# Optimization experiments

Measured on AMD Instinct MI355X. Metric: run time of the kernel, lower is better.

The kernel has to match this reference:

```python
import jax, jax.numpy as jnp
import numpy as np

N_NODES = 100000
N_EDGES = 1600000
IN_C, HID_C, OUT_C = 128, 256, 128


def setup_inputs() -> dict:
    key = jax.random.key(0)
    ks = jax.random.split(key, 6)
    x = jax.random.normal(ks[0], (N_NODES, IN_C), dtype=jnp.float32)
    edge_index = jax.random.randint(ks[1], (2, N_EDGES), 0, N_NODES, dtype=jnp.int64)
    s = 0.05
    W1a = jax.random.normal(ks[2], (IN_C, HID_C), dtype=jnp.float32) * s
    b1a = jnp.zeros((HID_C,), dtype=jnp.float32)
    W2a = jax.random.normal(ks[3], (HID_C, HID_C), dtype=jnp.float32) * s
    b2a = jnp.zeros((HID_C,), dtype=jnp.float32)
    W1b = jax.random.normal(ks[4], (HID_C, HID_C), dtype=jnp.float32) * s
    b1b = jnp.zeros((HID_C,), dtype=jnp.float32)
    W2b = jax.random.normal(ks[5], (HID_C, OUT_C), dtype=jnp.float32) * s
    b2b = jnp.zeros((OUT_C,), dtype=jnp.float32)
    return {"x": x, "edge_index": edge_index, "W1a": W1a, "b1a": b1a,
            "W2a": W2a, "b2a": b2a, "W1b": W1b, "b1b": b1b,
            "W2b": W2b, "b2b": b2b}


def _gin_conv(x, src, dst, W1, b1, W2, b2):
    # GINConv (eps=0): nn( x + sum_{j in N(i)} x_j )
    agg = jax.ops.segment_sum(x[src], dst, num_segments=N_NODES)  # [N, d]
    h = x + agg
    h = jnp.maximum(h @ W1 + b1, 0.0)
    return h @ W2 + b2


def reference(x, edge_index, W1a, b1a, W2a, b2a, W1b, b1b, W2b, b2b):
    src, dst = edge_index[0], edge_index[1]
    h = jnp.maximum(_gin_conv(x, src, dst, W1a, b1a, W2a, b2a), 0.0)  # relu(conv1)
    # dropout is identity in eval mode
    out = _gin_conv(h, src, dst, W1b, b1b, W2b, b2b)  # conv2
    return out
```

## Files before the change

kernel.cpp:

```cpp
#include <hip/hip_runtime.h>


#define N_NODES 100000
#define N_EDGES 1600000
#define NBUCK 13

typedef unsigned short ushort_t;
typedef short bf16x8 __attribute__((ext_vector_type(8)));
typedef float floatx4 __attribute__((ext_vector_type(4)));

static __device__ __forceinline__ ushort_t f2bf(float f) {
    unsigned u = __float_as_uint(f);
    u = (u + 0x7FFFu + ((u >> 16) & 1u)) >> 16;
    return (ushort_t)u;
}
static __device__ __forceinline__ unsigned pack2bf(float lo, float hi) {
    return (unsigned)f2bf(lo) | ((unsigned)f2bf(hi) << 16);
}
static __device__ __forceinline__ void addu4(float* acc, const uint4 v) {
    const unsigned w0 = v.x, w1 = v.y, w2 = v.z, w3 = v.w;
    acc[0] += __uint_as_float(w0 << 16);
    acc[1] += __uint_as_float(w0 & 0xFFFF0000u);
    acc[2] += __uint_as_float(w1 << 16);
    acc[3] += __uint_as_float(w1 & 0xFFFF0000u);
    acc[4] += __uint_as_float(w2 << 16);
    acc[5] += __uint_as_float(w2 & 0xFFFF0000u);
    acc[6] += __uint_as_float(w3 << 16);
    acc[7] += __uint_as_float(w3 & 0xFFFF0000u);
}

__global__ __launch_bounds__(256) void cvt_x_kernel(const float* __restrict__ X,
                                                    ushort_t* __restrict__ Xb, int n8) {
    int i = blockIdx.x * 256 + threadIdx.x;
    if (i < n8) {
        const float4 a = ((const float4*)X)[2 * i];
        const float4 b = ((const float4*)X)[2 * i + 1];
        uint4 r;
        r.x = pack2bf(a.x, a.y);
        r.y = pack2bf(a.z, a.w);
        r.z = pack2bf(b.x, b.y);
        r.w = pack2bf(b.z, b.w);
        ((uint4*)Xb)[i] = r;
    }
}

__global__ __launch_bounds__(256) void cvt_all_kernel(
    const float* __restrict__ W1a, const float* __restrict__ W2a,
    const float* __restrict__ W1b, const float* __restrict__ W2b,
    ushort_t* __restrict__ wt1a, ushort_t* __restrict__ wt2a,
    ushort_t* __restrict__ wt1b, ushort_t* __restrict__ wt2b) {
    int i = blockIdx.x * 256 + threadIdx.x;
    if (i < 32768) {
        int k = i >> 8, n = i & 255;
        wt1a[n * 128 + k] = f2bf(W1a[i]);
    } else if (i < 98304) {
        int j = i - 32768, k = j >> 8, n = j & 255;
        wt2a[n * 256 + k] = f2bf(W2a[j]);
    } else if (i < 163840) {
        int j = i - 98304, k = j >> 8, n = j & 255;
        wt1b[n * 256 + k] = f2bf(W1b[j]);
    } else if (i < 196608) {
        int j = i - 163840, k = j >> 7, n = j & 127;
        wt2b[n * 256 + k] = f2bf(W2b[j]);
    }
}

__global__ __launch_bounds__(256) void hist_kernel(const int* __restrict__ src,
                                                   const int* __restrict__ dst,
                                                   int* __restrict__ deg, int nE) {
    const int bucket = blockIdx.y;
    for (int e = blockIdx.x * 256 + threadIdx.x; e < nE; e += gridDim.x * 256) {
        int d = dst[e];
        int s = src[e];
        if ((unsigned)d < (unsigned)N_NODES && (unsigned)s < (unsigned)N_NODES &&
            (d >> 13) == bucket)
            atomicAdd(&deg[d], 1);
    }
}

__global__ __launch_bounds__(256) void fill_kernel(const int* __restrict__ src,
                                                   const int* __restrict__ dst,
                                                   int* __restrict__ cursor,
                                                   int* __restrict__ csr_src, int nE) {
    const int bucket = blockIdx.y;
    for (int e = blockIdx.x * 256 + threadIdx.x; e < nE; e += gridDim.x * 256) {
        int d = dst[e];
        int s = src[e];
        if ((unsigned)d < (unsigned)N_NODES && (unsigned)s < (unsigned)N_NODES &&
            (d >> 13) == bucket) {
            int pos = atomicAdd(&cursor[d], 1);
            csr_src[pos] = s;
        }
    }
}

__global__ __launch_bounds__(256) void scan1_kernel(const int* __restrict__ deg,
                                                    int* __restrict__ bsum, int n) {
    __shared__ int l[256];
    int b = blockIdx.x, t = threadIdx.x;
    int base = b * 1024 + t * 4;
    int s = 0;
#pragma unroll
    for (int k = 0; k < 4; ++k) {
        int i = base + k;
        if (i < n) s += deg[i];
    }
    l[t] = s;
    __syncthreads();
    for (int off = 128; off > 0; off >>= 1) {
        if (t < off) l[t] += l[t + off];
        __syncthreads();
    }
    if (t == 0) bsum[b] = l[0];
}

__global__ __launch_bounds__(128) void scan2_kernel(const int* __restrict__ bsum,
                                                    int* __restrict__ boff, int nb) {
    __shared__ int l[128];
    int t = threadIdx.x;
    int v = (t < nb) ? bsum[t] : 0;
    l[t] = v;
    __syncthreads();
    for (int off = 1; off < 128; off <<= 1) {
        int add = (t >= off) ? l[t - off] : 0;
        __syncthreads();
        l[t] += add;
        __syncthreads();
    }
    if (t < nb) boff[t] = l[t] - v;
}

__global__ __launch_bounds__(256) void scan3_kernel(const int* __restrict__ deg,
                                                    const int* __restrict__ boff,
                                                    int* __restrict__ row_ptr,
                                                    int* __restrict__ cursor, int n) {
    __shared__ int l[256];
    int b = blockIdx.x, t = threadIdx.x;
    int base = b * 1024 + t * 4;
    int d[4];
    int s = 0;
#pragma unroll
    for (int k = 0; k < 4; ++k) {
        int i = base + k;
        d[k] = (i < n) ? deg[i] : 0;
        s += d[k];
    }
    l[t] = s;
    __syncthreads();
    for (int off = 1; off < 256; off <<= 1) {
        int add = (t >= off) ? l[t - off] : 0;
        __syncthreads();
        l[t] += add;
        __syncthreads();
    }
    int run = boff[b] + l[t] - s;
#pragma unroll
    for (int k = 0; k < 4; ++k) {
        int i = base + k;
        if (i < n) {
            row_ptr[i] = run;
            cursor[i] = run;
        }
        run += d[k];
    }
}

template <int C>
__global__ __launch_bounds__(256) void agg_gather_kernel(
    const ushort_t* __restrict__ X, ushort_t* __restrict__ T,
    const int* __restrict__ row_ptr, const int* __restrict__ deg,
    const int* __restrict__ csr_src, int nN) {
    constexpr int G = C / 8;
    constexpr int NPW = 64 / G;
    const int lane = threadIdx.x & 63;
    const int wid = threadIdx.x >> 6;
    const int node = blockIdx.x * 4 + wid;
    if (node >= nN) return;
    const int sub = lane / G;
    const size_t coff = (size_t)(lane % G) * 8;

    float acc[8];
#pragma unroll
    for (int k = 0; k < 8; ++k) acc[k] = 0.f;

    const int base = row_ptr[node];
    const int dg = deg[node];
    for (int j0 = 0; j0 < dg; j0 += 64) {
        int cnt = dg - j0;
        if (cnt > 64) cnt = 64;
        int nidx = 0;
        if (lane < cnt) nidx = csr_src[base + j0 + lane];
        if ((unsigned)nidx >= (unsigned)N_NODES) nidx = 0;
        int j = 0;
        for (; j + 4 * NPW <= cnt; j += 4 * NPW) {
            uint4 v[4];
#pragma unroll
            for (int u = 0; u < 4; ++u) {
                int idx = __shfl(nidx, j + u * NPW + sub);
                v[u] = *(const uint4*)(X + (size_t)idx * C + coff);
            }
#pragma unroll
            for (int u = 0; u < 4; ++u) addu4(acc, v[u]);
        }
        for (; j < cnt; j += NPW) {
            int jj = j + sub;
            int srcl = (jj < cnt) ? jj : (cnt - 1);
            int idx = __shfl(nidx, srcl);
            if (jj < cnt) {
                uint4 v = *(const uint4*)(X + (size_t)idx * C + coff);
                addu4(acc, v);
            }
        }
    }
    if (sub == 0) {
        uint4 v = *(const uint4*)(X + (size_t)node * C + coff);
        addu4(acc, v);
    }
#pragma unroll
    for (int off = G; off < 64; off <<= 1)
#pragma unroll
        for (int k = 0; k < 8; ++k) acc[k] += __shfl_xor(acc[k], off);

    if (lane < G) {
        uint4 r;
        r.x = pack2bf(acc[0], acc[1]);
        r.y = pack2bf(acc[2], acc[3]);
        r.z = pack2bf(acc[4], acc[5]);
        r.w = pack2bf(acc[6], acc[7]);
        *(uint4*)(T + (size_t)node * C + coff) = r;
    }
}

template <bool RELU, typename OT>
__global__ __launch_bounds__(256) void gemm_kernel(
    const ushort_t* A, const ushort_t* __restrict__ Wt,
    const float* __restrict__ bias, OT* C, int M, int N, int K) {
    constexpr int BM = 128, BN = 128, BK = 32;
    constexpr int LDW = BK + 8;
    __shared__ ushort_t As[BM * LDW];
    __shared__ ushort_t Bs[BN * LDW];

    const int tid = threadIdx.x;
    const int lane = tid & 63;
    const int wid = tid >> 6;
    const int wm = wid & 1;
    const int wn = wid >> 1;
    const int l15 = lane & 15;
    const int q = lane >> 4;

    const int bm = blockIdx.x * BM;
    const int bn = blockIdx.y * BN;

    floatx4 acc[4][4];
#pragma unroll
    for (int mi = 0; mi < 4; ++mi)
#pragma unroll
        for (int ni = 0; ni < 4; ++ni) {
            floatx4 z = {0.f, 0.f, 0.f, 0.f};
            acc[mi][ni] = z;
        }

    for (int kt = 0; kt < K; kt += BK) {
#pragma unroll
        for (int p = 0; p < 4; ++p) {
            int i = p * 256 + tid;
            int row = i >> 3;
            int c4 = i & 7;
            int gr = bm + row;
            if (gr > M - 1) gr = M - 1;
            ushort4 u = *(const ushort4*)(A + (size_t)gr * K + kt + c4 * 4);
            *(ushort4*)&As[row * LDW + c4 * 4] = u;
        }
#pragma unroll
        for (int p = 0; p < 4; ++p) {
            int i = p * 256 + tid;
            int row = i >> 3;
            int c4 = i & 7;
            ushort4 u = *(const ushort4*)(Wt + (size_t)(bn + row) * K + kt + c4 * 4);
            *(ushort4*)&Bs[row * LDW + c4 * 4] = u;
        }
        __syncthreads();

        bf16x8 av[4], bv[4];
#pragma unroll
        for (int mi = 0; mi < 4; ++mi)
            av[mi] = *(const bf16x8*)&As[(wm * 64 + mi * 16 + l15) * LDW + q * 8];
#pragma unroll
        for (int ni = 0; ni < 4; ++ni)
            bv[ni] = *(const bf16x8*)&Bs[(wn * 64 + ni * 16 + l15) * LDW + q * 8];
#pragma unroll
        for (int mi = 0; mi < 4; ++mi)
#pragma unroll
            for (int ni = 0; ni < 4; ++ni)
                acc[mi][ni] = __builtin_amdgcn_mfma_f32_16x16x32_bf16(
                    av[mi], bv[ni], acc[mi][ni], 0, 0, 0);
        __syncthreads();
    }

    float bval[4];
#pragma unroll
    for (int ni = 0; ni < 4; ++ni) bval[ni] = bias[bn + wn * 64 + ni * 16 + l15];
#pragma unroll
    for (int mi = 0; mi < 4; ++mi) {
#pragma unroll
        for (int r = 0; r < 4; ++r) {
            int row = bm + wm * 64 + mi * 16 + q * 4 + r;
            if (row < M) {
#pragma unroll
                for (int ni = 0; ni < 4; ++ni) {
                    int col = bn + wn * 64 + ni * 16 + l15;
                    float v = acc[mi][ni][r] + bval[ni];
                    if (RELU) v = v > 0.f ? v : 0.f;
                    if constexpr (sizeof(OT) == 2)
                        C[(size_t)row * N + col] = f2bf(v);
                    else
                        C[(size_t)row * N + col] = v;
                }
            }
        }
    }
}

extern "C" void kernel_launch(void* const* d_in, const int* in_sizes, int n_in,
                              void* d_out, int out_size, void* d_ws, size_t ws_size,
                              hipStream_t stream) {
    const float* x   = (const float*)d_in[0];
    const int*   ei  = (const int*)d_in[1];
    const float* W1a = (const float*)d_in[2];
    const float* b1a = (const float*)d_in[3];
    const float* W2a = (const float*)d_in[4];
    const float* b2a = (const float*)d_in[5];
    const float* W1b = (const float*)d_in[6];
    const float* b1b = (const float*)d_in[7];
    const float* W2b = (const float*)d_in[8];
    const float* b2b = (const float*)d_in[9];
    const int* src = ei;
    const int* dst = ei + N_EDGES;
    float* out = (float*)d_out;

    char* base = (char*)d_ws;
    size_t o = 0;
    ushort_t* wt1a = (ushort_t*)(base + o); o += 128 * 256 * 2;
    ushort_t* wt2a = (ushort_t*)(base + o); o += 256 * 256 * 2;
    ushort_t* wt1b = (ushort_t*)(base + o); o += 256 * 256 * 2;
    ushort_t* wt2b = (ushort_t*)(base + o); o += 256 * 128 * 2;
    o = (o + 255) & ~(size_t)255;
    int* deg     = (int*)(base + o); o += (size_t)N_NODES * 4;
    int* row_ptr = (int*)(base + o); o += (size_t)N_NODES * 4;
    int* cursor  = (int*)(base + o); o += (size_t)N_NODES * 4;
    int* bsum    = (int*)(base + o); o += 128 * 4;
    int* boff    = (int*)(base + o); o += 128 * 4;
    o = (o + 255) & ~(size_t)255;
    int* csr_src = (int*)(base + o); o += (size_t)N_EDGES * 4;
    o = (o + 255) & ~(size_t)255;
    ushort_t* t1   = (ushort_t*)(base + o); o += (size_t)N_NODES * 128 * 2;
    ushort_t* tbig = (ushort_t*)(base + o); o += (size_t)N_NODES * 256 * 2;
    (void)ws_size; (void)o; (void)in_sizes; (void)n_in; (void)out_size;

    ushort_t* inter = (ushort_t*)d_out;
    ushort_t* xb    = (ushort_t*)d_out;

    cvt_all_kernel<<<768, 256, 0, stream>>>(W1a, W2a, W1b, W2b,
                                            wt1a, wt2a, wt1b, wt2b);
    cvt_x_kernel<<<(N_NODES * 128 / 8 + 255) / 256, 256, 0, stream>>>(
        x, xb, N_NODES * 128 / 8);

    const int NB = (N_NODES + 1023) / 1024;
    hipMemsetAsync(deg, 0, (size_t)N_NODES * 4, stream);
    hist_kernel<<<dim3(1024, NBUCK), 256, 0, stream>>>(src, dst, deg, N_EDGES);
    scan1_kernel<<<NB, 256, 0, stream>>>(deg, bsum, N_NODES);
    scan2_kernel<<<1, 128, 0, stream>>>(bsum, boff, NB);
    scan3_kernel<<<NB, 256, 0, stream>>>(deg, boff, row_ptr, cursor, N_NODES);
    fill_kernel<<<dim3(1024, NBUCK), 256, 0, stream>>>(src, dst, cursor, csr_src,
                                                       N_EDGES);

    const int gm = (N_NODES + 127) / 128;
    const int ga = (N_NODES + 3) / 4;

    agg_gather_kernel<128><<<ga, 256, 0, stream>>>(xb, t1, row_ptr, deg,
                                                   csr_src, N_NODES);
    gemm_kernel<true, ushort_t><<<dim3(gm, 2), 256, 0, stream>>>(
        t1, wt1a, b1a, tbig, N_NODES, 256, 128);
    gemm_kernel<true, ushort_t><<<dim3(gm, 2), 256, 0, stream>>>(
        tbig, wt2a, b2a, inter, N_NODES, 256, 256);

    agg_gather_kernel<256><<<ga, 256, 0, stream>>>(inter, tbig, row_ptr,
                                                   deg, csr_src, N_NODES);
    gemm_kernel<true, ushort_t><<<dim3(gm, 2), 256, 0, stream>>>(
        tbig, wt1b, b1b, inter, N_NODES, 256, 256);
    gemm_kernel<false, float><<<dim3(gm, 1), 256, 0, stream>>>(
        inter, wt2b, b2b, out, N_NODES, 128, 256);
}
```

Before: 590.8 us.

## Use direct global-to-LDS loads in GEMM and predicated zero-row gather unrolling

The GEMM tile loads now use global_load_lds (16-byte direct global-to-LDS transfers) with an unpadded LDS layout. This removes the register round-trip and the ds_write instructions but gives up the padding that avoided bank conflicts on the MFMA fragment reads. The aggregation kernel drops its tail loop: out-of-range neighbors read from a zeroed dummy row, and the unroll factor is a template parameter (4 for 128 channels, 8 for 256). Together these aim for more loads in flight per wave, at the cost of some wasted loads on low-degree nodes.

```diff
diff --git a/kernel.cpp b/kernel.cpp
--- a/kernel.cpp
+++ b/kernel.cpp
@@ -28,6 +28,11 @@
     acc[6] += __uint_as_float(w3 << 16);
     acc[7] += __uint_as_float(w3 & 0xFFFF0000u);
 }
+
+#define GLOAD_LDS16(g, l)                                                     \
+    __builtin_amdgcn_global_load_lds(                                         \
+        (const __attribute__((address_space(1))) void*)(g),                   \
+        (__attribute__((address_space(3))) void*)(l), 16, 0, 0)
 
 __global__ __launch_bounds__(256) void cvt_x_kernel(const float* __restrict__ X,
                                                     ushort_t* __restrict__ Xb, int n8) {
@@ -165,19 +170,20 @@
     }
 }
 
-template <int C>
+template <int C, int U>
 __global__ __launch_bounds__(256) void agg_gather_kernel(
     const ushort_t* __restrict__ X, ushort_t* __restrict__ T,
     const int* __restrict__ row_ptr, const int* __restrict__ deg,
-    const int* __restrict__ csr_src, int nN) {
+    const int* __restrict__ csr_src, const ushort_t* __restrict__ zrow, int nN) {
     constexpr int G = C / 8;
     constexpr int NPW = 64 / G;
+    constexpr int B = U * NPW;
     const int lane = threadIdx.x & 63;
     const int wid = threadIdx.x >> 6;
     const int node = blockIdx.x * 4 + wid;
     if (node >= nN) return;
     const int sub = lane / G;
-    const size_t coff = (size_t)(lane % G) * 8;
+    const int coff = (lane % G) * 8;
 
     float acc[8];
 #pragma unroll
@@ -188,28 +194,20 @@
     for (int j0 = 0; j0 < dg; j0 += 64) {
         int cnt = dg - j0;
         if (cnt > 64) cnt = 64;
-        int nidx = 0;
-        if (lane < cnt) nidx = csr_src[base + j0 + lane];
+        int nidx = (lane < cnt) ? csr_src[base + j0 + lane] : 0;
         if ((unsigned)nidx >= (unsigned)N_NODES) nidx = 0;
-        int j = 0;
-        for (; j + 4 * NPW <= cnt; j += 4 * NPW) {
-            uint4 v[4];
-#pragma unroll
-            for (int u = 0; u < 4; ++u) {
-                int idx = __shfl(nidx, j + u * NPW + sub);
-                v[u] = *(const uint4*)(X + (size_t)idx * C + coff);
+        for (int j = 0; j < cnt; j += B) {
+            uint4 v[U];
+#pragma unroll
+            for (int u = 0; u < U; ++u) {
+                int jj = j + u * NPW + sub;
+                bool ok = jj < cnt;
+                int idx = __shfl(nidx, ok ? jj : 0);
+                const ushort_t* p = ok ? (X + (size_t)idx * C) : zrow;
+                v[u] = *(const uint4*)(p + coff);
             }
 #pragma unroll
-            for (int u = 0; u < 4; ++u) addu4(acc, v[u]);
-        }
-        for (; j < cnt; j += NPW) {
-            int jj = j + sub;
-            int srcl = (jj < cnt) ? jj : (cnt - 1);
-            int idx = __shfl(nidx, srcl);
-            if (jj < cnt) {
-                uint4 v = *(const uint4*)(X + (size_t)idx * C + coff);
-                addu4(acc, v);
-            }
+            for (int u = 0; u < U; ++u) addu4(acc, v[u]);
         }
     }
     if (sub == 0) {
@@ -236,9 +234,8 @@
     const ushort_t* A, const ushort_t* __restrict__ Wt,
     const float* __restrict__ bias, OT* C, int M, int N, int K) {
     constexpr int BM = 128, BN = 128, BK = 32;
-    constexpr int LDW = BK + 8;
-    __shared__ ushort_t As[BM * LDW];
-    __shared__ ushort_t Bs[BN * LDW];
+    __shared__ ushort_t As[BM * BK];
+    __shared__ ushort_t Bs[BN * BK];
 
     const int tid = threadIdx.x;
     const int lane = tid & 63;
@@ -247,6 +244,8 @@
     const int wn = wid >> 1;
     const int l15 = lane & 15;
     const int q = lane >> 4;
+    const int srow = lane >> 2;
+    const int scol = (lane & 3) * 8;
 
     const int bm = blockIdx.x * BM;
     const int bn = blockIdx.y * BN;
@@ -262,32 +261,25 @@
 
     for (int kt = 0; kt < K; kt += BK) {
 #pragma unroll
-        for (int p = 0; p < 4; ++p) {
-            int i = p * 256 + tid;
-            int row = i >> 3;
-            int c4 = i & 7;
-            int gr = bm + row;
-            if (gr > M - 1) gr = M - 1;
-            ushort4 u = *(const ushort4*)(A + (size_t)gr * K + kt + c4 * 4);
-            *(ushort4*)&As[row * LDW + c4 * 4] = u;
-        }
-#pragma unroll
-        for (int p = 0; p < 4; ++p) {
-            int i = p * 256 + tid;
-            int row = i >> 3;
-            int c4 = i & 7;
-            ushort4 u = *(const ushort4*)(Wt + (size_t)(bn + row) * K + kt + c4 * 4);
-            *(ushort4*)&Bs[row * LDW + c4 * 4] = u;
+        for (int half = 0; half < 2; ++half) {
+            const int row = wid * 32 + half * 16 + srow;
+            const int gr = bm + row;
+            const ushort_t* gpa = A + (size_t)gr * K + kt + scol;
+            ushort_t* lpa = &As[(wid * 32 + half * 16) * BK];
+            if (gr < M) GLOAD_LDS16(gpa, lpa);
+            const ushort_t* gpb = Wt + (size_t)(bn + row) * K + kt + scol;
+            ushort_t* lpb = &Bs[(wid * 32 + half * 16) * BK];
+            GLOAD_LDS16(gpb, lpb);
         }
         __syncthreads();
 
         bf16x8 av[4], bv[4];
 #pragma unroll
         for (int mi = 0; mi < 4; ++mi)
-            av[mi] = *(const bf16x8*)&As[(wm * 64 + mi * 16 + l15) * LDW + q * 8];
+            av[mi] = *(const bf16x8*)&As[(wm * 64 + mi * 16 + l15) * BK + q * 8];
 #pragma unroll
         for (int ni = 0; ni < 4; ++ni)
-            bv[ni] = *(const bf16x8*)&Bs[(wn * 64 + ni * 16 + l15) * LDW + q * 8];
+            bv[ni] = *(const bf16x8*)&Bs[(wn * 64 + ni * 16 + l15) * BK + q * 8];
 #pragma unroll
         for (int mi = 0; mi < 4; ++mi)
 #pragma unroll
@@ -345,6 +337,7 @@
     ushort_t* wt1b = (ushort_t*)(base + o); o += 256 * 256 * 2;
     ushort_t* wt2b = (ushort_t*)(base + o); o += 256 * 128 * 2;
     o = (o + 255) & ~(size_t)255;
+    ushort_t* zrow = (ushort_t*)(base + o); o += 512;
     int* deg     = (int*)(base + o); o += (size_t)N_NODES * 4;
     int* row_ptr = (int*)(base + o); o += (size_t)N_NODES * 4;
     int* cursor  = (int*)(base + o); o += (size_t)N_NODES * 4;
@@ -355,6 +348,7 @@
     o = (o + 255) & ~(size_t)255;
     ushort_t* t1   = (ushort_t*)(base + o); o += (size_t)N_NODES * 128 * 2;
     ushort_t* tbig = (ushort_t*)(base + o); o += (size_t)N_NODES * 256 * 2;
+    o += 128 * 1024;
     (void)ws_size; (void)o; (void)in_sizes; (void)n_in; (void)out_size;
 
     ushort_t* inter = (ushort_t*)d_out;
@@ -366,7 +360,7 @@
         x, xb, N_NODES * 128 / 8);
 
     const int NB = (N_NODES + 1023) / 1024;
-    hipMemsetAsync(deg, 0, (size_t)N_NODES * 4, stream);
+    hipMemsetAsync(zrow, 0, 512 + (size_t)N_NODES * 4, stream);
     hist_kernel<<<dim3(1024, NBUCK), 256, 0, stream>>>(src, dst, deg, N_EDGES);
     scan1_kernel<<<NB, 256, 0, stream>>>(deg, bsum, N_NODES);
     scan2_kernel<<<1, 128, 0, stream>>>(bsum, boff, NB);
@@ -377,15 +371,15 @@
     const int gm = (N_NODES + 127) / 128;
     const int ga = (N_NODES + 3) / 4;
 
-    agg_gather_kernel<128><<<ga, 256, 0, stream>>>(xb, t1, row_ptr, deg,
-                                                   csr_src, N_NODES);
+    agg_gather_kernel<128, 4><<<ga, 256, 0, stream>>>(xb, t1, row_ptr, deg,
+                                                      csr_src, zrow, N_NODES);
     gemm_kernel<true, ushort_t><<<dim3(gm, 2), 256, 0, stream>>>(
         t1, wt1a, b1a, tbig, N_NODES, 256, 128);
     gemm_kernel<true, ushort_t><<<dim3(gm, 2), 256, 0, stream>>>(
         tbig, wt2a, b2a, inter, N_NODES, 256, 256);
 
-    agg_gather_kernel<256><<<ga, 256, 0, stream>>>(inter, tbig, row_ptr,
-                                                   deg, csr_src, N_NODES);
+    agg_gather_kernel<256, 8><<<ga, 256, 0, stream>>>(inter, tbig, row_ptr,
+                                                      deg, csr_src, zrow, N_NODES);
     gemm_kernel<true, ushort_t><<<dim3(gm, 2), 256, 0, stream>>>(
         tbig, wt1b, b1b, inter, N_NODES, 256, 256);
     gemm_kernel<false, float><<<dim3(gm, 1), 256, 0, stream>>>(
```

Measured after the change: 578.1 us. 2.1% less time.
